# Kernel optimization log

Measured on AMD Instinct MI355X. Metric: run time of the kernel, lower is better.

Reference implementation:

```python
import jax, jax.numpy as jnp
import numpy as np

B = 2048        # batch (== window_size so the buggy subtraction loop covers all time steps)
WIN = 2048      # window_size
E = 64          # emb_dim


def setup_inputs() -> dict:
    key = jax.random.key(0)
    k0, k1, k2, k3, k4 = jax.random.split(key, 5)
    x = jax.random.normal(k0, (B, WIN, E), dtype=jnp.float32)
    W1 = jax.random.normal(k1, (E, WIN), dtype=jnp.float32) / np.sqrt(WIN).astype(np.float32)
    b1 = jax.random.normal(k2, (E,), dtype=jnp.float32) * 0.01
    # Linear2(emb_dim -> 1)
    W2 = jax.random.normal(k3, (E, 1), dtype=jnp.float32) / np.sqrt(E).astype(np.float32)
    b2 = jax.random.normal(k4, (1,), dtype=jnp.float32) * 0.01
    return {"x": x, "W1": W1, "b1": b1, "W2": W2, "b2": b2}


def reference(x, W1, b1, W2, b2):
    # seq_last is detached in the original torch code
    seq_last = jax.lax.stop_gradient(x[:, -1, :])          # [B, E]
    x_adj = x - seq_last[:, None, :]                       # subtract last step from every time step
    # per-channel matvec: out[b,e] = sum_w x_adj[b,w,e] * W1[e,w] + b1[e]
    out = jnp.einsum('bwe,ew->be', x_adj, W1) + b1 + seq_last  # [B, E]
    return out @ W2 + b2                                   # [B, 1]
```

## Files before the change

kernel.cpp:

```cpp
#include <hip/hip_runtime.h>

#define WINSZ 2048
#define EMB   64

__global__ __launch_bounds__(256) void nl_precompute_c(
    const float* __restrict__ W1, const float* __restrict__ b1,
    const float* __restrict__ W2, const float* __restrict__ b2,
    float* __restrict__ c, float* __restrict__ Cconst)
{
    const int e = blockIdx.x;
    const int t = threadIdx.x;

    float s = 0.0f;
    for (int w = t; w < WINSZ; w += 256) s += W1[e * WINSZ + w];

    for (int off = 32; off; off >>= 1) s += __shfl_down(s, off, 64);

    __shared__ float sm[4];
    const int lane = t & 63, wid = t >> 6;
    if (lane == 0) sm[wid] = s;
    __syncthreads();

    if (t == 0) {
        const float S1 = sm[0] + sm[1] + sm[2] + sm[3];
        c[e] = W2[e] * (1.0f - S1);
    }
    if (e == 0 && t == 0) {
        float acc = b2[0];
        #pragma unroll
        for (int i = 0; i < EMB; ++i) acc = fmaf(W2[i], b1[i], acc);
        *Cconst = acc;
    }
}

__global__ __launch_bounds__(256) void nl_build_V(
    const float* __restrict__ W1, const float* __restrict__ W2,
    const float* __restrict__ c, float* __restrict__ V)
{
    const int i = blockIdx.x * 256 + threadIdx.x;
    if (i >= WINSZ * EMB) return;
    const int w = i >> 6;
    const int e = i & (EMB - 1);
    float v = W1[e * WINSZ + w] * W2[e];
    if (w == WINSZ - 1) v += c[e];
    V[i] = v;
}

__global__ __launch_bounds__(256) void nl_main(
    const float* __restrict__ x, const float* __restrict__ V,
    const float* __restrict__ Cconst, float* __restrict__ out)
{
    const int b = blockIdx.x;
    const int t = threadIdx.x;

    const float4* __restrict__ xp = (const float4*)(x + (size_t)b * (WINSZ * EMB));
    const float4* __restrict__ vp = (const float4*)V;

    float acc = 0.0f;
    constexpr int N4 = (WINSZ * EMB) / 4;
    #pragma unroll 4
    for (int j = t; j < N4; j += 256) {
        const float4 xv = xp[j];
        const float4 vv = vp[j];
        acc = fmaf(xv.x, vv.x, acc);
        acc = fmaf(xv.y, vv.y, acc);
        acc = fmaf(xv.z, vv.z, acc);
        acc = fmaf(xv.w, vv.w, acc);
    }

    for (int off = 32; off; off >>= 1) acc += __shfl_down(acc, off, 64);

    __shared__ float sm[4];
    const int lane = t & 63, wid = t >> 6;
    if (lane == 0) sm[wid] = acc;
    __syncthreads();

    if (t == 0) out[b] = sm[0] + sm[1] + sm[2] + sm[3] + *Cconst;
}

extern "C" void kernel_launch(void* const* d_in, const int* in_sizes, int n_in,
                              void* d_out, int out_size, void* d_ws, size_t ws_size,
                              hipStream_t stream)
{
    const float* x  = (const float*)d_in[0];
    const float* W1 = (const float*)d_in[1];
    const float* b1 = (const float*)d_in[2];
    const float* W2 = (const float*)d_in[3];
    const float* b2 = (const float*)d_in[4];
    float* out = (float*)d_out;

    float* V  = (float*)d_ws;
    float* c  = V + WINSZ * EMB;
    float* Cc = c + EMB;

    const int B = out_size;

    nl_precompute_c<<<EMB, 256, 0, stream>>>(W1, b1, W2, b2, c, Cc);
    nl_build_V<<<(WINSZ * EMB + 255) / 256, 256, 0, stream>>>(W1, W2, c, V);
    nl_main<<<B, 256, 0, stream>>>(x, V, Cc, out);
}
```

Baseline: 199.2 us.

## Fuse V precompute kernels and process two batch rows per block with nontemporal loads

Merges the column-sum and V-building kernels into one launch that keeps W1 values in registers. The main kernel now handles two batch rows per block, so each V load is reused for both rows, and it uses four independent vector accumulators. x is streamed with nontemporal loads to avoid polluting cache. This halves the block count, and the V writes in the fused precompute are strided (non-coalesced).

Measured after the change: 169.9 us (median of 2 runs). 1.17x faster.

```diff
diff --git a/kernel.cpp b/kernel.cpp
--- a/kernel.cpp
+++ b/kernel.cpp
@@ -3,16 +3,24 @@
 #define WINSZ 2048
 #define EMB   64
 
-__global__ __launch_bounds__(256) void nl_precompute_c(
+typedef float f32x4 __attribute__((ext_vector_type(4)));
+
+__global__ __launch_bounds__(256) void nl_precompute(
     const float* __restrict__ W1, const float* __restrict__ b1,
     const float* __restrict__ W2, const float* __restrict__ b2,
-    float* __restrict__ c, float* __restrict__ Cconst)
+    float* __restrict__ V, float* __restrict__ Cconst)
 {
     const int e = blockIdx.x;
     const int t = threadIdx.x;
 
+    float vals[WINSZ / 256];
     float s = 0.0f;
-    for (int w = t; w < WINSZ; w += 256) s += W1[e * WINSZ + w];
+    #pragma unroll
+    for (int k = 0; k < WINSZ / 256; ++k) {
+        const int w = t + k * 256;
+        vals[k] = W1[e * WINSZ + w];
+        s += vals[k];
+    }
 
     for (int off = 32; off; off >>= 1) s += __shfl_down(s, off, 64);
 
@@ -21,10 +29,18 @@
     if (lane == 0) sm[wid] = s;
     __syncthreads();
 
-    if (t == 0) {
-        const float S1 = sm[0] + sm[1] + sm[2] + sm[3];
-        c[e] = W2[e] * (1.0f - S1);
+    const float S1 = sm[0] + sm[1] + sm[2] + sm[3];
+    const float w2 = W2[e];
+    const float ce = w2 * (1.0f - S1);
+
+    #pragma unroll
+    for (int k = 0; k < WINSZ / 256; ++k) {
+        const int w = t + k * 256;
+        float v = vals[k] * w2;
+        if (w == WINSZ - 1) v += ce;
+        V[w * EMB + e] = v;
     }
+
     if (e == 0 && t == 0) {
         float acc = b2[0];
         #pragma unroll
@@ -33,49 +49,56 @@
     }
 }
 
-__global__ __launch_bounds__(256) void nl_build_V(
-    const float* __restrict__ W1, const float* __restrict__ W2,
-    const float* __restrict__ c, float* __restrict__ V)
-{
-    const int i = blockIdx.x * 256 + threadIdx.x;
-    if (i >= WINSZ * EMB) return;
-    const int w = i >> 6;
-    const int e = i & (EMB - 1);
-    float v = W1[e * WINSZ + w] * W2[e];
-    if (w == WINSZ - 1) v += c[e];
-    V[i] = v;
-}
-
 __global__ __launch_bounds__(256) void nl_main(
     const float* __restrict__ x, const float* __restrict__ V,
     const float* __restrict__ Cconst, float* __restrict__ out)
 {
-    const int b = blockIdx.x;
-    const int t = threadIdx.x;
+    const int b0 = blockIdx.x * 2;
+    const int t  = threadIdx.x;
 
-    const float4* __restrict__ xp = (const float4*)(x + (size_t)b * (WINSZ * EMB));
-    const float4* __restrict__ vp = (const float4*)V;
+    constexpr int N4 = (WINSZ * EMB) / 4;
 
-    float acc = 0.0f;
-    constexpr int N4 = (WINSZ * EMB) / 4;
-    #pragma unroll 4
-    for (int j = t; j < N4; j += 256) {
-        const float4 xv = xp[j];
-        const float4 vv = vp[j];
-        acc = fmaf(xv.x, vv.x, acc);
-        acc = fmaf(xv.y, vv.y, acc);
-        acc = fmaf(xv.z, vv.z, acc);
-        acc = fmaf(xv.w, vv.w, acc);
+    const f32x4* __restrict__ xp0 = (const f32x4*)(x + (size_t)b0 * (WINSZ * EMB));
+    const f32x4* __restrict__ xp1 = xp0 + N4;
+    const f32x4* __restrict__ vp  = (const f32x4*)V;
+
+    f32x4 a00 = {0,0,0,0}, a01 = {0,0,0,0};
+    f32x4 a10 = {0,0,0,0}, a11 = {0,0,0,0};
+
+    for (int j0 = 0; j0 < N4; j0 += 512) {
+        const int j = j0 + t;
+        const f32x4 xA0 = __builtin_nontemporal_load(xp0 + j);
+        const f32x4 xA1 = __builtin_nontemporal_load(xp0 + j + 256);
+        const f32x4 xB0 = __builtin_nontemporal_load(xp1 + j);
+        const f32x4 xB1 = __builtin_nontemporal_load(xp1 + j + 256);
+        const f32x4 v0  = vp[j];
+        const f32x4 v1  = vp[j + 256];
+        a00 += xA0 * v0;
+        a01 += xA1 * v1;
+        a10 += xB0 * v0;
+        a11 += xB1 * v1;
     }
 
-    for (int off = 32; off; off >>= 1) acc += __shfl_down(acc, off, 64);
+    const f32x4 aA = a00 + a01;
+    const f32x4 aB = a10 + a11;
+    float r0 = (aA.x + aA.y) + (aA.z + aA.w);
+    float r1 = (aB.x + aB.y) + (aB.z + aB.w);
 
-    __shared__ float sm[4];
+    for (int off = 32; off; off >>= 1) {
+        r0 += __shfl_down(r0, off, 64);
+        r1 += __shfl_down(r1, off, 64);
+    }
+
+    __shared__ float smA[4], smB[4];
     const int lane = t & 63, wid = t >> 6;
-    if (lane == 0) sm[wid] = acc;
+    if (lane == 0) { smA[wid] = r0; smB[wid] = r1; }
     __syncthreads();
 
-    if (t == 0) out[b] = sm[0] + sm[1] + sm[2] + sm[3] + *Cconst;
+    if (t == 0) {
+        const float C = *Cconst;
+        out[b0]     = smA[0] + smA[1] + smA[2] + smA[3] + C;
+        out[b0 + 1] = smB[0] + smB[1] + smB[2] + smB[3] + C;
+    }
 }
 
 extern "C" void kernel_launch(void* const* d_in, const int* in_sizes, int n_in,
@@ -90,12 +113,10 @@
     float* out = (float*)d_out;
 
     float* V  = (float*)d_ws;
-    float* c  = V + WINSZ * EMB;
-    float* Cc = c + EMB;
+    float* Cc = V + WINSZ * EMB;
 
     const int B = out_size;
 
-    nl_precompute_c<<<EMB, 256, 0, stream>>>(W1, b1, W2, b2, c, Cc);
-    nl_build_V<<<(WINSZ * EMB + 255) / 256, 256, 0, stream>>>(W1, W2, c, V);
-    nl_main<<<B, 256, 0, stream>>>(x, V, Cc, out);
+    nl_precompute<<<EMB, 256, 0, stream>>>(W1, b1, W2, b2, V, Cc);
+    nl_main<<<B / 2, 256, 0, stream>>>(x, V, Cc, out);
 }
```
